# Optimization experiments

Hardware: AMD Instinct MI355X
Metric: run time of the kernel (lower is better)

The kernel has to match this reference:

```python
import jax, jax.numpy as jnp
import numpy as np

NUM_EXPERTS = 8
TOP_K = 2
LB_WEIGHT = 0.01
LN_EPS = 1e-5


def setup_inputs() -> dict:
    key = jax.random.key(0)
    ks = jax.random.split(key, 4)
    B, S, D, H, E = 4, 2048, 1024, 2048, NUM_EXPERTS
    x = jax.random.normal(ks[0], (B, S, D), dtype=jnp.float32)
    gate_w = jax.random.normal(ks[1], (E, D), dtype=jnp.float32) * 0.02
    w1 = jax.random.normal(ks[2], (E, H, D), dtype=jnp.float32) * 0.02
    w2 = jax.random.normal(ks[3], (E, D, H), dtype=jnp.float32) * 0.02
    ln_gamma = jnp.ones((D,), dtype=jnp.float32)
    ln_beta = jnp.zeros((D,), dtype=jnp.float32)
    return {"x": x, "gate_w": gate_w, "w1": w1, "w2": w2,
            "ln_gamma": ln_gamma, "ln_beta": ln_beta}


def reference(x, gate_w, w1, w2, ln_gamma, ln_beta):
    residual = x
    # LayerNorm (eval mode, dropout=0)
    mu = jnp.mean(x, axis=-1, keepdims=True)
    var = jnp.var(x, axis=-1, keepdims=True)
    xn = (x - mu) * jax.lax.rsqrt(var + LN_EPS) * ln_gamma + ln_beta

    # Router: logits [B,S,E], top-k gating with softmax over selected logits
    logits = jnp.einsum('bsd,ed->bse', xn, gate_w)
    top_vals, top_idx = jax.lax.top_k(logits, TOP_K)  # [B,S,K]
    gates = jax.nn.softmax(top_vals, axis=-1)

    # Load-balance aux loss: (std/mean)^2 of mean routing probs (torch std -> ddof=1)
    probs = jax.nn.softmax(logits, axis=-1)
    avg_probs = jnp.mean(probs, axis=(0, 1))  # [E]
    lb_loss = (jnp.std(avg_probs, ddof=1) / (jnp.mean(avg_probs) + 1e-6)) ** 2

    # Expert dispatch/combine: small fixed loop over experts; tokens not
    # routed to expert e get combined gate 0, matching the torch scatter.
    out = jnp.zeros_like(xn)
    for e in range(NUM_EXPERTS):
        ge = jnp.sum(gates * (top_idx == e), axis=-1)  # [B,S]
        h = jax.nn.gelu(jnp.einsum('bsd,hd->bsh', xn, w1[e]), approximate=False)
        y = jnp.einsum('bsh,dh->bsd', h, w2[e])
        out = out + y * ge[..., None]

    return residual + out, lb_loss * LB_WEIGHT
```

## Files before the change

kernel.cpp:

```cpp
#include <hip/hip_runtime.h>

#define T_TOK 8192
#define DIM 1024
#define HID 2048
#define NE 8
#define TK 16384

typedef __bf16 bf16x8 __attribute__((ext_vector_type(8)));
typedef float f32x4 __attribute__((ext_vector_type(4)));

#define OFF_XN      0UL
#define OFF_W1B     16777216UL
#define OFF_W2B     50331648UL
#define OFF_H       83886080UL
#define OFF_ATOK    150994944UL
#define OFF_INV     151060480UL
#define OFF_TOPI    151126016UL
#define OFF_GATES   151158784UL
#define OFF_CPART   151224320UL
#define OFF_PPART   151226368UL
#define OFF_COUNTS  151228416UL
#define OFF_OFFS    151228448UL
#define OFF_CNT2    151228480UL
#define OFF_NT      151228512UL
#define OFF_TMAP    151228544UL

__device__ __forceinline__ unsigned short f2bf(float f) {
    union { float fv; unsigned u; } q; q.fv = f;
    unsigned r = q.u + 0x7fffu + ((q.u >> 16) & 1u);
    return (unsigned short)(r >> 16);
}

__device__ __forceinline__ float bf2f(unsigned short u) {
    union { unsigned u; float f; } q; q.u = ((unsigned)u) << 16;
    return q.f;
}

__device__ __forceinline__ float gelu_exact(float x) {
    return 0.5f * x * (1.0f + erff(x * 0.70710678118654752440f));
}

__device__ __forceinline__ int sw(int r) { return (r ^ (r >> 2)) & 3; }

__device__ __forceinline__ void g2l16(const unsigned short* g, unsigned short* l) {
    __builtin_amdgcn_global_load_lds(
        (const __attribute__((address_space(1))) unsigned int*)g,
        (__attribute__((address_space(3))) unsigned int*)l, 16, 0, 0);
}

__global__ __launch_bounds__(256) void convert_kernel(const float4* __restrict__ src,
                                                      ushort4* __restrict__ dst, int n4) {
    int i = blockIdx.x * 256 + threadIdx.x;
    if (i < n4) {
        float4 f = src[i];
        ushort4 u;
        u.x = f2bf(f.x); u.y = f2bf(f.y); u.z = f2bf(f.z); u.w = f2bf(f.w);
        dst[i] = u;
    }
}

__global__ __launch_bounds__(256) void ln_router_kernel(
    const float* __restrict__ x, const float* __restrict__ gw,
    const float* __restrict__ gamma, const float* __restrict__ beta,
    unsigned short* __restrict__ xnb, int* __restrict__ top_idx,
    float2* __restrict__ gates, int* __restrict__ counts_partial,
    float* __restrict__ probs_partial)
{
    __shared__ float sprob[8];
    __shared__ int scnt[8];
    int tid = threadIdx.x;
    if (tid < 8) { sprob[tid] = 0.f; scnt[tid] = 0; }
    __syncthreads();

    int wave = tid >> 6, lane = tid & 63;
    int t = blockIdx.x * 4 + wave;
    const float* xt = x + (size_t)t * DIM;

    float v[16];
    float s = 0.f, sq = 0.f;
#pragma unroll
    for (int j = 0; j < 4; j++) {
        float4 f = *(const float4*)(xt + j * 256 + lane * 4);
        v[4*j+0] = f.x; v[4*j+1] = f.y; v[4*j+2] = f.z; v[4*j+3] = f.w;
        s += f.x + f.y + f.z + f.w;
        sq += f.x*f.x + f.y*f.y + f.z*f.z + f.w*f.w;
    }
#pragma unroll
    for (int o = 32; o > 0; o >>= 1) { s += __shfl_xor(s, o); sq += __shfl_xor(sq, o); }
    float mean = s * (1.0f / DIM);
    float var = sq * (1.0f / DIM) - mean * mean;
    float rstd = rsqrtf(var + 1e-5f);

#pragma unroll
    for (int j = 0; j < 4; j++) {
        float4 gm = *(const float4*)(gamma + j * 256 + lane * 4);
        float4 bt = *(const float4*)(beta + j * 256 + lane * 4);
        float x0 = (v[4*j+0] - mean) * rstd * gm.x + bt.x;
        float x1 = (v[4*j+1] - mean) * rstd * gm.y + bt.y;
        float x2 = (v[4*j+2] - mean) * rstd * gm.z + bt.z;
        float x3 = (v[4*j+3] - mean) * rstd * gm.w + bt.w;
        ushort4 u; u.x = f2bf(x0); u.y = f2bf(x1); u.z = f2bf(x2); u.w = f2bf(x3);
        *(ushort4*)(xnb + (size_t)t * DIM + j * 256 + lane * 4) = u;
        v[4*j+0] = x0; v[4*j+1] = x1; v[4*j+2] = x2; v[4*j+3] = x3;
    }

    double part[8];
#pragma unroll
    for (int e = 0; e < 8; e++) {
        double p = 0.0;
        const float* ge = gw + (size_t)e * DIM;
#pragma unroll
        for (int j = 0; j < 4; j++) {
            float4 g = *(const float4*)(ge + j * 256 + lane * 4);
            p += (double)v[4*j+0] * (double)g.x;
            p += (double)v[4*j+1] * (double)g.y;
            p += (double)v[4*j+2] * (double)g.z;
            p += (double)v[4*j+3] * (double)g.w;
        }
        part[e] = p;
    }
#pragma unroll
    for (int o = 32; o > 0; o >>= 1)
#pragma unroll
        for (int e = 0; e < 8; e++) part[e] += __shfl_xor(part[e], o);

    if (lane == 0) {
        double l0 = -1e300; int e0 = -1;
#pragma unroll
        for (int e = 0; e < 8; e++) if (part[e] > l0) { l0 = part[e]; e0 = e; }
        double l1 = -1e300; int e1 = -1;
#pragma unroll
        for (int e = 0; e < 8; e++) if (e != e0 && part[e] > l1) { l1 = part[e]; e1 = e; }
        float d = expf((float)(l1 - l0));
        float g0 = 1.0f / (1.0f + d);
        float g1 = d / (1.0f + d);
        top_idx[t] = e0 | (e1 << 8);
        gates[t] = make_float2(g0, g1);
        atomicAdd(&scnt[e0], 1);
        atomicAdd(&scnt[e1], 1);
        float pe[8]; float sum = 0.f;
#pragma unroll
        for (int e = 0; e < 8; e++) { pe[e] = expf((float)(part[e] - l0)); sum += pe[e]; }
        float inv = 1.0f / sum;
#pragma unroll
        for (int e = 0; e < 8; e++) atomicAdd(&sprob[e], pe[e] * inv);
    }
    __syncthreads();
    if (tid < 8) {
        int bin = (blockIdx.x & 63) * 8 + tid;
        atomicAdd(&probs_partial[bin], sprob[tid]);
        atomicAdd(&counts_partial[bin], scnt[tid]);
    }
}

__global__ void finalize_kernel(const int* __restrict__ counts_partial,
                                const float* __restrict__ probs_partial,
                                int* __restrict__ counts, int* __restrict__ offsets,
                                int* __restrict__ cnt2, int* __restrict__ ntiles,
                                int4* __restrict__ tile_map, float* __restrict__ lb_out)
{
    if (threadIdx.x != 0 || blockIdx.x != 0) return;
    int c[8]; float p[8];
    for (int e = 0; e < 8; e++) { c[e] = 0; p[e] = 0.f; }
    for (int b = 0; b < 64; b++)
        for (int e = 0; e < 8; e++) { c[e] += counts_partial[b*8+e]; p[e] += probs_partial[b*8+e]; }
    int off = 0, nt = 0;
    for (int e = 0; e < 8; e++) {
        offsets[e] = off; counts[e] = c[e]; cnt2[e] = 0;
        for (int m0 = 0; m0 < c[e]; m0 += 128) tile_map[nt++] = make_int4(e, m0, off, c[e]);
        off += c[e];
    }
    *ntiles = nt;
    float avg[8]; float m = 0.f;
    for (int e = 0; e < 8; e++) { avg[e] = p[e] / (float)T_TOK; m += avg[e]; }
    m *= (1.0f / 8.0f);
    float var = 0.f;
    for (int e = 0; e < 8; e++) { float d = avg[e] - m; var += d * d; }
    var *= (1.0f / 7.0f);
    float mm = m + 1e-6f;
    lb_out[0] = (var / (mm * mm)) * 0.01f;
}

__global__ __launch_bounds__(256) void placement_kernel(
    const int* __restrict__ top_idx,
    const int* __restrict__ offsets, int* __restrict__ cnt2,
    int* __restrict__ atok, int2* __restrict__ inv)
{
    __shared__ int lcnt[8];
    __shared__ int lbase[8];
    __shared__ int ltok[4096];
    int tid = threadIdx.x;
    if (tid < 8) lcnt[tid] = 0;
    __syncthreads();
    int t = blockIdx.x * 256 + tid;
    int pk = top_idx[t];
    int e0 = pk & 255, e1 = (pk >> 8) & 255;
    int p0 = atomicAdd(&lcnt[e0], 1); ltok[e0*512+p0] = t;
    int p1 = atomicAdd(&lcnt[e1], 1); ltok[e1*512+p1] = t;
    __syncthreads();
    if (tid < 8) lbase[tid] = offsets[tid] + atomicAdd(&cnt2[tid], lcnt[tid]);
    __syncthreads();
    for (int e = 0; e < 8; e++) {
        int c = lcnt[e], b = lbase[e];
        for (int i = tid; i < c; i += 256) atok[b+i] = ltok[e*512+i];
    }
    inv[t] = make_int2(lbase[e0] + p0, lbase[e1] + p1);
}

__global__ __launch_bounds__(256) void gemm1_kernel(
    const unsigned short* __restrict__ xnb, const unsigned short* __restrict__ w1b,
    unsigned short* __restrict__ hbuf, const int* __restrict__ atok,
    const int4* __restrict__ tile_map, const int* __restrict__ ntiles)
{
    if ((int)blockIdx.x >= *ntiles) return;
    int4 tm = tile_map[blockIdx.x];
    int e = tm.x, m0 = tm.y, base = tm.z, cnt = tm.w;
    int n0 = blockIdx.y * 128;

    __shared__ unsigned short As[128 * 32];
    __shared__ unsigned short Bs[128 * 32];

    int tid = threadIdx.x;
    int lane = tid & 63, wave = tid >> 6;

    int r0 = tid >> 2, r1 = 64 + (tid >> 2), seg = tid & 3;
    int a0i = base + m0 + r0; if (m0 + r0 >= cnt) a0i = base;
    int a1i = base + m0 + r1; if (m0 + r1 >= cnt) a1i = base;
    int tok0 = atok[a0i], tok1 = atok[a1i];
    const unsigned short* ap0 = xnb + (size_t)tok0 * DIM + (seg ^ sw(r0)) * 8;
    const unsigned short* ap1 = xnb + (size_t)tok1 * DIM + (seg ^ sw(r1)) * 8;
    const unsigned short* bp0 = w1b + ((size_t)e * HID + n0 + r0) * DIM + (seg ^ sw(r0)) * 8;
    const unsigned short* bp1 = w1b + ((size_t)e * HID + n0 + r1) * DIM + (seg ^ sw(r1)) * 8;
    unsigned short* lA0 = &As[(size_t)tid * 8];
    unsigned short* lA1 = &As[(size_t)(256 + tid) * 8];
    unsigned short* lB0 = &Bs[(size_t)tid * 8];
    unsigned short* lB1 = &Bs[(size_t)(256 + tid) * 8];

    int wm = (wave >> 1) * 64, wn = (wave & 1) * 64;
    int quad = lane >> 4, col = lane & 15;
    int aoff[4], boff[4];
#pragma unroll
    for (int i = 0; i < 4; i++) {
        int m = wm + i * 16 + col;
        aoff[i] = m * 32 + ((quad ^ sw(m)) * 8);
        int n = wn + i * 16 + col;
        boff[i] = n * 32 + ((quad ^ sw(n)) * 8);
    }

    f32x4 acc[4][4] = {};
    for (int k0 = 0; k0 < DIM; k0 += 32) {
        __syncthreads();
        g2l16(ap0 + k0, lA0);
        g2l16(ap1 + k0, lA1);
        g2l16(bp0 + k0, lB0);
        g2l16(bp1 + k0, lB1);
        __syncthreads();
        bf16x8 a[4], b[4];
#pragma unroll
        for (int i = 0; i < 4; i++) a[i] = *(const bf16x8*)&As[aoff[i]];
#pragma unroll
        for (int i = 0; i < 4; i++) b[i] = *(const bf16x8*)&Bs[boff[i]];
#pragma unroll
        for (int mi = 0; mi < 4; mi++)
#pragma unroll
            for (int ni = 0; ni < 4; ni++)
                acc[mi][ni] = __builtin_amdgcn_mfma_f32_16x16x32_bf16(a[mi], b[ni], acc[mi][ni], 0, 0, 0);
    }

#pragma unroll
    for (int mi = 0; mi < 4; mi++)
#pragma unroll
        for (int i = 0; i < 4; i++) {
            int m = wm + mi * 16 + quad * 4 + i;
            if (m0 + m < cnt) {
                size_t hrow = (size_t)(base + m0 + m) * HID + n0;
#pragma unroll
                for (int ni = 0; ni < 4; ni++)
                    hbuf[hrow + wn + ni * 16 + col] = f2bf(gelu_exact(acc[mi][ni][i]));
            }
        }
}

__global__ __launch_bounds__(256) void gemm2_kernel(
    const unsigned short* __restrict__ hbuf, const unsigned short* __restrict__ w2b,
    unsigned short* __restrict__ ybuf,
    const int4* __restrict__ tile_map, const int* __restrict__ ntiles)
{
    if ((int)blockIdx.x >= *ntiles) return;
    int4 tm = tile_map[blockIdx.x];
    int e = tm.x, m0 = tm.y, base = tm.z, cnt = tm.w;
    int n0 = blockIdx.y * 128;

    __shared__ unsigned short As[128 * 32];
    __shared__ unsigned short Bs[128 * 32];

    int tid = threadIdx.x;
    int lane = tid & 63, wave = tid >> 6;

    int r0 = tid >> 2, r1 = 64 + (tid >> 2), seg = tid & 3;
    int a0i = base + m0 + r0; if (m0 + r0 >= cnt) a0i = base;
    int a1i = base + m0 + r1; if (m0 + r1 >= cnt) a1i = base;
    const unsigned short* ap0 = hbuf + (size_t)a0i * HID + (seg ^ sw(r0)) * 8;
    const unsigned short* ap1 = hbuf + (size_t)a1i * HID + (seg ^ sw(r1)) * 8;
    const unsigned short* bp0 = w2b + ((size_t)e * DIM + n0 + r0) * HID + (seg ^ sw(r0)) * 8;
    const unsigned short* bp1 = w2b + ((size_t)e * DIM + n0 + r1) * HID + (seg ^ sw(r1)) * 8;
    unsigned short* lA0 = &As[(size_t)tid * 8];
    unsigned short* lA1 = &As[(size_t)(256 + tid) * 8];
    unsigned short* lB0 = &Bs[(size_t)tid * 8];
    unsigned short* lB1 = &Bs[(size_t)(256 + tid) * 8];

    int wm = (wave >> 1) * 64, wn = (wave & 1) * 64;
    int quad = lane >> 4, col = lane & 15;
    int aoff[4], boff[4];
#pragma unroll
    for (int i = 0; i < 4; i++) {
        int m = wm + i * 16 + col;
        aoff[i] = m * 32 + ((quad ^ sw(m)) * 8);
        int n = wn + i * 16 + col;
        boff[i] = n * 32 + ((quad ^ sw(n)) * 8);
    }

    f32x4 acc[4][4] = {};
    for (int k0 = 0; k0 < HID; k0 += 32) {
        __syncthreads();
        g2l16(ap0 + k0, lA0);
        g2l16(ap1 + k0, lA1);
        g2l16(bp0 + k0, lB0);
        g2l16(bp1 + k0, lB1);
        __syncthreads();
        bf16x8 a[4], b[4];
#pragma unroll
        for (int i = 0; i < 4; i++) a[i] = *(const bf16x8*)&As[aoff[i]];
#pragma unroll
        for (int i = 0; i < 4; i++) b[i] = *(const bf16x8*)&Bs[boff[i]];
#pragma unroll
        for (int mi = 0; mi < 4; mi++)
#pragma unroll
            for (int ni = 0; ni < 4; ni++)
                acc[mi][ni] = __builtin_amdgcn_mfma_f32_16x16x32_bf16(a[mi], b[ni], acc[mi][ni], 0, 0, 0);
    }

#pragma unroll
    for (int mi = 0; mi < 4; mi++)
#pragma unroll
        for (int i = 0; i < 4; i++) {
            int m = wm + mi * 16 + quad * 4 + i;
            if (m0 + m < cnt) {
                size_t yrow = (size_t)(base + m0 + m) * DIM + n0;
#pragma unroll
                for (int ni = 0; ni < 4; ni++)
                    ybuf[yrow + wn + ni * 16 + col] = f2bf(acc[mi][ni][i]);
            }
        }
}

__global__ __launch_bounds__(256) void combine_kernel(
    const float* __restrict__ x, const unsigned short* __restrict__ ybuf,
    const int2* __restrict__ inv, const float2* __restrict__ gates,
    float* __restrict__ out)
{
    int tid = threadIdx.x;
    int wave = tid >> 6, lane = tid & 63;
    int t = blockIdx.x * 4 + wave;
    int2 sl = inv[t];
    float2 g = gates[t];
    const float* xr = x + (size_t)t * DIM;
    const unsigned short* y0 = ybuf + (size_t)sl.x * DIM;
    const unsigned short* y1 = ybuf + (size_t)sl.y * DIM;
    float* orow = out + (size_t)t * DIM;
#pragma unroll
    for (int j = 0; j < 4; j++) {
        int idx = j * 256 + lane * 4;
        float4 xv = *(const float4*)(xr + idx);
        ushort4 a = *(const ushort4*)(y0 + idx);
        ushort4 b = *(const ushort4*)(y1 + idx);
        float4 o;
        o.x = xv.x + g.x * bf2f(a.x) + g.y * bf2f(b.x);
        o.y = xv.y + g.x * bf2f(a.y) + g.y * bf2f(b.y);
        o.z = xv.z + g.x * bf2f(a.z) + g.y * bf2f(b.z);
        o.w = xv.w + g.x * bf2f(a.w) + g.y * bf2f(b.w);
        *(float4*)(orow + idx) = o;
    }
}

extern "C" void kernel_launch(void* const* d_in, const int* in_sizes, int n_in,
                              void* d_out, int out_size, void* d_ws, size_t ws_size,
                              hipStream_t stream) {
    (void)in_sizes; (void)n_in; (void)out_size; (void)ws_size;
    const float* x     = (const float*)d_in[0];
    const float* gw    = (const float*)d_in[1];
    const float* w1    = (const float*)d_in[2];
    const float* w2    = (const float*)d_in[3];
    const float* gamma = (const float*)d_in[4];
    const float* beta  = (const float*)d_in[5];
    float* out = (float*)d_out;
    char* ws = (char*)d_ws;

    unsigned short* xnb  = (unsigned short*)(ws + OFF_XN);
    unsigned short* w1b  = (unsigned short*)(ws + OFF_W1B);
    unsigned short* w2b  = (unsigned short*)(ws + OFF_W2B);
    unsigned short* hbuf = (unsigned short*)(ws + OFF_H);
    unsigned short* ybuf = (unsigned short*)(ws + OFF_W1B);
    int*    atok    = (int*)(ws + OFF_ATOK);
    int2*   inv     = (int2*)(ws + OFF_INV);
    int*    topi    = (int*)(ws + OFF_TOPI);
    float2* gates   = (float2*)(ws + OFF_GATES);
    int*    cpart   = (int*)(ws + OFF_CPART);
    float*  ppart   = (float*)(ws + OFF_PPART);
    int*    counts  = (int*)(ws + OFF_COUNTS);
    int*    offsets = (int*)(ws + OFF_OFFS);
    int*    cnt2    = (int*)(ws + OFF_CNT2);
    int*    ntiles  = (int*)(ws + OFF_NT);
    int4*   tmap    = (int4*)(ws + OFF_TMAP);

    hipMemsetAsync(ws + OFF_CPART, 0, 4096, stream);

    convert_kernel<<<16384, 256, 0, stream>>>((const float4*)w1, (ushort4*)w1b, (NE*HID*DIM)/4);
    convert_kernel<<<16384, 256, 0, stream>>>((const float4*)w2, (ushort4*)w2b, (NE*DIM*HID)/4);

    ln_router_kernel<<<T_TOK / 4, 256, 0, stream>>>(x, gw, gamma, beta, xnb, topi, gates, cpart, ppart);
    finalize_kernel<<<1, 64, 0, stream>>>(cpart, ppart, counts, offsets, cnt2, ntiles, tmap,
                                          out + (size_t)T_TOK * DIM);
    placement_kernel<<<T_TOK / 256, 256, 0, stream>>>(topi, offsets, cnt2, atok, inv);

    gemm1_kernel<<<dim3(136, HID / 128), 256, 0, stream>>>(xnb, w1b, hbuf, atok, tmap, ntiles);
    gemm2_kernel<<<dim3(136, DIM / 128), 256, 0, stream>>>(hbuf, w2b, ybuf, tmap, ntiles);
    combine_kernel<<<T_TOK / 4, 256, 0, stream>>>(x, ybuf, inv, gates, out);
}
```

Measured before the change: 466.6 us.

## Double GEMM K-tile, merge weight conversions, parallelize finalize, use tanh GELU

Both expert GEMMs now stage a 64-wide K slice per barrier pair, with an 8-way XOR swizzle, so each sync covers twice the MFMA work. The two weight-conversion launches are merged into one, and the finalize reduction now uses wave shuffles instead of a single-thread loop. The exact erf GELU is replaced with a tanh approximation built from exp and rcp. That changes numerics relative to the exact-GELU reference and may break tolerance.

```diff
diff --git a/kernel.cpp b/kernel.cpp
--- a/kernel.cpp
+++ b/kernel.cpp
@@ -36,11 +36,15 @@
     return q.f;
 }
 
-__device__ __forceinline__ float gelu_exact(float x) {
-    return 0.5f * x * (1.0f + erff(x * 0.70710678118654752440f));
-}
-
-__device__ __forceinline__ int sw(int r) { return (r ^ (r >> 2)) & 3; }
+__device__ __forceinline__ float gelu_fast(float x) {
+    float x3 = x * x * x;
+    float z2 = 1.5957691216f * (x + 0.044715f * x3);
+    float u = __expf(z2);
+    float t = 1.0f - 2.0f * __builtin_amdgcn_rcpf(u + 1.0f);
+    return 0.5f * x * (1.0f + t);
+}
+
+__device__ __forceinline__ int sw8(int r) { return (r ^ (r >> 3)) & 7; }
 
 __device__ __forceinline__ void g2l16(const unsigned short* g, unsigned short* l) {
     __builtin_amdgcn_global_load_lds(
@@ -48,14 +52,22 @@
         (__attribute__((address_space(3))) unsigned int*)l, 16, 0, 0);
 }
 
-__global__ __launch_bounds__(256) void convert_kernel(const float4* __restrict__ src,
-                                                      ushort4* __restrict__ dst, int n4) {
+__global__ __launch_bounds__(256) void convert_kernel(
+    const float4* __restrict__ s1, ushort4* __restrict__ d1, int n1,
+    const float4* __restrict__ s2, ushort4* __restrict__ d2, int n2)
+{
     int i = blockIdx.x * 256 + threadIdx.x;
-    if (i < n4) {
-        float4 f = src[i];
-        ushort4 u;
-        u.x = f2bf(f.x); u.y = f2bf(f.y); u.z = f2bf(f.z); u.w = f2bf(f.w);
-        dst[i] = u;
+    if (i < n1) {
+        float4 f = s1[i];
+        ushort4 u; u.x = f2bf(f.x); u.y = f2bf(f.y); u.z = f2bf(f.z); u.w = f2bf(f.w);
+        d1[i] = u;
+    } else {
+        int j = i - n1;
+        if (j < n2) {
+            float4 f = s2[j];
+            ushort4 u; u.x = f2bf(f.x); u.y = f2bf(f.y); u.z = f2bf(f.z); u.w = f2bf(f.w);
+            d2[j] = u;
+        }
     }
 }
 
@@ -159,26 +171,32 @@
                                 int* __restrict__ cnt2, int* __restrict__ ntiles,
                                 int4* __restrict__ tile_map, float* __restrict__ lb_out)
 {
-    if (threadIdx.x != 0 || blockIdx.x != 0) return;
+    int tid = threadIdx.x;
     int c[8]; float p[8];
-    for (int e = 0; e < 8; e++) { c[e] = 0; p[e] = 0.f; }
-    for (int b = 0; b < 64; b++)
-        for (int e = 0; e < 8; e++) { c[e] += counts_partial[b*8+e]; p[e] += probs_partial[b*8+e]; }
-    int off = 0, nt = 0;
-    for (int e = 0; e < 8; e++) {
-        offsets[e] = off; counts[e] = c[e]; cnt2[e] = 0;
-        for (int m0 = 0; m0 < c[e]; m0 += 128) tile_map[nt++] = make_int4(e, m0, off, c[e]);
-        off += c[e];
-    }
-    *ntiles = nt;
-    float avg[8]; float m = 0.f;
-    for (int e = 0; e < 8; e++) { avg[e] = p[e] / (float)T_TOK; m += avg[e]; }
-    m *= (1.0f / 8.0f);
-    float var = 0.f;
-    for (int e = 0; e < 8; e++) { float d = avg[e] - m; var += d * d; }
-    var *= (1.0f / 7.0f);
-    float mm = m + 1e-6f;
-    lb_out[0] = (var / (mm * mm)) * 0.01f;
+#pragma unroll
+    for (int e = 0; e < 8; e++) { c[e] = counts_partial[tid*8+e]; p[e] = probs_partial[tid*8+e]; }
+#pragma unroll
+    for (int o = 32; o > 0; o >>= 1)
+#pragma unroll
+        for (int e = 0; e < 8; e++) { c[e] += __shfl_xor(c[e], o); p[e] += __shfl_xor(p[e], o); }
+
+    if (tid == 0) {
+        int off = 0, nt = 0;
+        for (int e = 0; e < 8; e++) {
+            offsets[e] = off; counts[e] = c[e]; cnt2[e] = 0;
+            for (int m0 = 0; m0 < c[e]; m0 += 128) tile_map[nt++] = make_int4(e, m0, off, c[e]);
+            off += c[e];
+        }
+        *ntiles = nt;
+        float avg[8]; float m = 0.f;
+        for (int e = 0; e < 8; e++) { avg[e] = p[e] / (float)T_TOK; m += avg[e]; }
+        m *= (1.0f / 8.0f);
+        float var = 0.f;
+        for (int e = 0; e < 8; e++) { float d = avg[e] - m; var += d * d; }
+        var *= (1.0f / 7.0f);
+        float mm = m + 1e-6f;
+        lb_out[0] = (var / (mm * mm)) * 0.01f;
+    }
 }
 
 __global__ __launch_bounds__(256) void placement_kernel(
@@ -217,54 +235,59 @@
     int e = tm.x, m0 = tm.y, base = tm.z, cnt = tm.w;
     int n0 = blockIdx.y * 128;
 
-    __shared__ unsigned short As[128 * 32];
-    __shared__ unsigned short Bs[128 * 32];
-
-    int tid = threadIdx.x;
-    int lane = tid & 63, wave = tid >> 6;
-
-    int r0 = tid >> 2, r1 = 64 + (tid >> 2), seg = tid & 3;
-    int a0i = base + m0 + r0; if (m0 + r0 >= cnt) a0i = base;
-    int a1i = base + m0 + r1; if (m0 + r1 >= cnt) a1i = base;
-    int tok0 = atok[a0i], tok1 = atok[a1i];
-    const unsigned short* ap0 = xnb + (size_t)tok0 * DIM + (seg ^ sw(r0)) * 8;
-    const unsigned short* ap1 = xnb + (size_t)tok1 * DIM + (seg ^ sw(r1)) * 8;
-    const unsigned short* bp0 = w1b + ((size_t)e * HID + n0 + r0) * DIM + (seg ^ sw(r0)) * 8;
-    const unsigned short* bp1 = w1b + ((size_t)e * HID + n0 + r1) * DIM + (seg ^ sw(r1)) * 8;
-    unsigned short* lA0 = &As[(size_t)tid * 8];
-    unsigned short* lA1 = &As[(size_t)(256 + tid) * 8];
-    unsigned short* lB0 = &Bs[(size_t)tid * 8];
-    unsigned short* lB1 = &Bs[(size_t)(256 + tid) * 8];
+    __shared__ unsigned short As[128 * 64];
+    __shared__ unsigned short Bs[128 * 64];
+
+    int tid = threadIdx.x, lane = tid & 63, wave = tid >> 6;
+    int sg = tid & 7;
+
+    const unsigned short* ap[4];
+    const unsigned short* bp[4];
+#pragma unroll
+    for (int j = 0; j < 4; j++) {
+        int r = j * 32 + (tid >> 3);
+        int ai = base + m0 + r; if (m0 + r >= cnt) ai = base;
+        int tok = atok[ai];
+        int ss = (sg ^ sw8(r)) * 8;
+        ap[j] = xnb + (size_t)tok * DIM + ss;
+        bp[j] = w1b + ((size_t)e * HID + n0 + r) * DIM + ss;
+    }
 
     int wm = (wave >> 1) * 64, wn = (wave & 1) * 64;
     int quad = lane >> 4, col = lane & 15;
-    int aoff[4], boff[4];
-#pragma unroll
-    for (int i = 0; i < 4; i++) {
-        int m = wm + i * 16 + col;
-        aoff[i] = m * 32 + ((quad ^ sw(m)) * 8);
-        int n = wn + i * 16 + col;
-        boff[i] = n * 32 + ((quad ^ sw(n)) * 8);
-    }
+    int aoff[4][2], boff[4][2];
+#pragma unroll
+    for (int i = 0; i < 4; i++)
+#pragma unroll
+        for (int s = 0; s < 2; s++) {
+            int m = wm + i * 16 + col;
+            aoff[i][s] = m * 64 + ((((s << 2) | quad) ^ sw8(m)) * 8);
+            int n = wn + i * 16 + col;
+            boff[i][s] = n * 64 + ((((s << 2) | quad) ^ sw8(n)) * 8);
+        }
 
     f32x4 acc[4][4] = {};
-    for (int k0 = 0; k0 < DIM; k0 += 32) {
+    for (int k0 = 0; k0 < DIM; k0 += 64) {
         __syncthreads();
-        g2l16(ap0 + k0, lA0);
-        g2l16(ap1 + k0, lA1);
-        g2l16(bp0 + k0, lB0);
-        g2l16(bp1 + k0, lB1);
+#pragma unroll
+        for (int j = 0; j < 4; j++) {
+            g2l16(ap[j] + k0, &As[(j * 256 + tid) * 8]);
+            g2l16(bp[j] + k0, &Bs[(j * 256 + tid) * 8]);
+        }
         __syncthreads();
-        bf16x8 a[4], b[4];
-#pragma unroll
-        for (int i = 0; i < 4; i++) a[i] = *(const bf16x8*)&As[aoff[i]];
-#pragma unroll
-        for (int i = 0; i < 4; i++) b[i] = *(const bf16x8*)&Bs[boff[i]];
-#pragma unroll
-        for (int mi = 0; mi < 4; mi++)
-#pragma unroll
-            for (int ni = 0; ni < 4; ni++)
-                acc[mi][ni] = __builtin_amdgcn_mfma_f32_16x16x32_bf16(a[mi], b[ni], acc[mi][ni], 0, 0, 0);
+#pragma unroll
+        for (int s = 0; s < 2; s++) {
+            bf16x8 a[4], b[4];
+#pragma unroll
+            for (int i = 0; i < 4; i++) a[i] = *(const bf16x8*)&As[aoff[i][s]];
+#pragma unroll
+            for (int i = 0; i < 4; i++) b[i] = *(const bf16x8*)&Bs[boff[i][s]];
+#pragma unroll
+            for (int mi = 0; mi < 4; mi++)
+#pragma unroll
+                for (int ni = 0; ni < 4; ni++)
+                    acc[mi][ni] = __builtin_amdgcn_mfma_f32_16x16x32_bf16(a[mi], b[ni], acc[mi][ni], 0, 0, 0);
+        }
     }
 
 #pragma unroll
@@ -276,7 +299,7 @@
                 size_t hrow = (size_t)(base + m0 + m) * HID + n0;
 #pragma unroll
                 for (int ni = 0; ni < 4; ni++)
-                    hbuf[hrow + wn + ni * 16 + col] = f2bf(gelu_exact(acc[mi][ni][i]));
+                    hbuf[hrow + wn + ni * 16 + col] = f2bf(gelu_fast(acc[mi][ni][i]));
             }
         }
 }
@@ -291,53 +314,58 @@
     int e = tm.x, m0 = tm.y, base = tm.z, cnt = tm.w;
     int n0 = blockIdx.y * 128;
 
-    __shared__ unsigned short As[128 * 32];
-    __shared__ unsigned short Bs[128 * 32];
-
-    int tid = threadIdx.x;
-    int lane = tid & 63, wave = tid >> 6;
-
-    int r0 = tid >> 2, r1 = 64 + (tid >> 2), seg = tid & 3;
-    int a0i = base + m0 + r0; if (m0 + r0 >= cnt) a0i = base;
-    int a1i = base + m0 + r1; if (m0 + r1 >= cnt) a1i = base;
-    const unsigned short* ap0 = hbuf + (size_t)a0i * HID + (seg ^ sw(r0)) * 8;
-    const unsigned short* ap1 = hbuf + (size_t)a1i * HID + (seg ^ sw(r1)) * 8;
-    const unsigned short* bp0 = w2b + ((size_t)e * DIM + n0 + r0) * HID + (seg ^ sw(r0)) * 8;
-    const unsigned short* bp1 = w2b + ((size_t)e * DIM + n0 + r1) * HID + (seg ^ sw(r1)) * 8;
-    unsigned short* lA0 = &As[(size_t)tid * 8];
-    unsigned short* lA1 = &As[(size_t)(256 + tid) * 8];
-    unsigned short* lB0 = &Bs[(size_t)tid * 8];
-    unsigned short* lB1 = &Bs[(size_t)(256 + tid) * 8];
+    __shared__ unsigned short As[128 * 64];
+    __shared__ unsigned short Bs[128 * 64];
+
+    int tid = threadIdx.x, lane = tid & 63, wave = tid >> 6;
+    int sg = tid & 7;
+
+    const unsigned short* ap[4];
+    const unsigned short* bp[4];
+#pragma unroll
+    for (int j = 0; j < 4; j++) {
+        int r = j * 32 + (tid >> 3);
+        int ai = base + m0 + r; if (m0 + r >= cnt) ai = base;
+        int ss = (sg ^ sw8(r)) * 8;
+        ap[j] = hbuf + (size_t)ai * HID + ss;
+        bp[j] = w2b + ((size_t)e * DIM + n0 + r) * HID + ss;
+    }
 
     int wm = (wave >> 1) * 64, wn = (wave & 1) * 64;
     int quad = lane >> 4, col = lane & 15;
-    int aoff[4], boff[4];
-#pragma unroll
-    for (int i = 0; i < 4; i++) {
-        int m = wm + i * 16 + col;
-        aoff[i] = m * 32 + ((quad ^ sw(m)) * 8);
-        int n = wn + i * 16 + col;
-        boff[i] = n * 32 + ((quad ^ sw(n)) * 8);
-    }
+    int aoff[4][2], boff[4][2];
+#pragma unroll
+    for (int i = 0; i < 4; i++)
+#pragma unroll
+        for (int s = 0; s < 2; s++) {
+            int m = wm + i * 16 + col;
+            aoff[i][s] = m * 64 + ((((s << 2) | quad) ^ sw8(m)) * 8);
+            int n = wn + i * 16 + col;
+            boff[i][s] = n * 64 + ((((s << 2) | quad) ^ sw8(n)) * 8);
+        }
 
     f32x4 acc[4][4] = {};
-    for (int k0 = 0; k0 < HID; k0 += 32) {
+    for (int k0 = 0; k0 < HID; k0 += 64) {
         __syncthreads();
-        g2l16(ap0 + k0, lA0);
-        g2l16(ap1 + k0, lA1);
-        g2l16(bp0 + k0, lB0);
-        g2l16(bp1 + k0, lB1);
+#pragma unroll
+        for (int j = 0; j < 4; j++) {
+            g2l16(ap[j] + k0, &As[(j * 256 + tid) * 8]);
+            g2l16(bp[j] + k0, &Bs[(j * 256 + tid) * 8]);
+        }
         __syncthreads();
-        bf16x8 a[4], b[4];
-#pragma unroll
-        for (int i = 0; i < 4; i++) a[i] = *(const bf16x8*)&As[aoff[i]];
-#pragma unroll
-        for (int i = 0; i < 4; i++) b[i] = *(const bf16x8*)&Bs[boff[i]];
-#pragma unroll
-        for (int mi = 0; mi < 4; mi++)
-#pragma unroll
-            for (int ni = 0; ni < 4; ni++)
-                acc[mi][ni] = __builtin_amdgcn_mfma_f32_16x16x32_bf16(a[mi], b[ni], acc[mi][ni], 0, 0, 0);
+#pragma unroll
+        for (int s = 0; s < 2; s++) {
+            bf16x8 a[4], b[4];
+#pragma unroll
+            for (int i = 0; i < 4; i++) a[i] = *(const bf16x8*)&As[aoff[i][s]];
+#pragma unroll
+            for (int i = 0; i < 4; i++) b[i] = *(const bf16x8*)&Bs[boff[i][s]];
+#pragma unroll
+            for (int mi = 0; mi < 4; mi++)
+#pragma unroll
+                for (int ni = 0; ni < 4; ni++)
+                    acc[mi][ni] = __builtin_amdgcn_mfma_f32_16x16x32_bf16(a[mi], b[ni], acc[mi][ni], 0, 0, 0);
+        }
     }
 
 #pragma unroll
@@ -415,8 +443,9 @@
 
     hipMemsetAsync(ws + OFF_CPART, 0, 4096, stream);
 
-    convert_kernel<<<16384, 256, 0, stream>>>((const float4*)w1, (ushort4*)w1b, (NE*HID*DIM)/4);
-    convert_kernel<<<16384, 256, 0, stream>>>((const float4*)w2, (ushort4*)w2b, (NE*DIM*HID)/4);
+    int n1 = (NE * HID * DIM) / 4, n2 = (NE * DIM * HID) / 4;
+    convert_kernel<<<(n1 + n2 + 255) / 256, 256, 0, stream>>>(
+        (const float4*)w1, (ushort4*)w1b, n1, (const float4*)w2, (ushort4*)w2b, n2);
 
     ln_router_kernel<<<T_TOK / 4, 256, 0, stream>>>(x, gw, gamma, beta, xnb, topi, gates, cpart, ppart);
     finalize_kernel<<<1, 64, 0, stream>>>(cpart, ppart, counts, offsets, cnt2, ntiles, tmap,
```

After: 448.5 us. 3.9% less time.
